# Performance work log

Measured on AMD Instinct MI355X. Metric: run time of the kernel, lower is better.

The kernel has to match this reference:

```python
import jax, jax.numpy as jnp
import numpy as np

N = 100000      # nodes
E = 1600000     # edges (avg degree 16)
DIN = 48        # input features
H = 48          # hidden
DOUT = 16       # output classes


def setup_inputs() -> dict:
    key = jax.random.key(0)
    ks = jax.random.split(key, 20)
    inp = {
        "x": jax.random.normal(ks[0], (N, DIN), jnp.float32),
        "edge_index": jax.random.randint(ks[1], (2, E), 0, N, jnp.int32),
    }
    # (name, in_dim, out_dim) for the 2-layer MLP in each of 3 GINConvs + final fc
    layers = [("11", DIN, H), ("12", H, H),
              ("21", H, H), ("22", H, H),
              ("31", H, H), ("32", H, H),
              ("f1", H, H), ("f2", H, DOUT)]
    for i, (nm, din, dout) in enumerate(layers):
        inp["w" + nm] = jax.random.normal(ks[2 + i], (din, dout), jnp.float32) / np.float32(np.sqrt(din))
        inp["b" + nm] = jax.random.normal(ks[10 + i], (dout,), jnp.float32) * 0.01
    return inp


def reference(x, edge_index, w11, b11, w12, b12, w21, b21, w22, b22,
              w31, b31, w32, b32, wf1, bf1, wf2, bf2):
    src, dst = edge_index[0], edge_index[1]
    n = x.shape[0]

    def gin_conv(h, w1, b1, w2, b2):
        # scatter-sum neighbor aggregation: sum_{j in N(i)} h_j
        agg = jax.ops.segment_sum(h[src], dst, num_segments=n)  # [N, d]
        h2 = h + agg  # eps = 0 (PyG GINConv default): (1+eps)*x + agg
        h2 = jax.nn.relu(h2 @ w1 + b1)
        return jax.nn.relu(h2 @ w2 + b2)

    h = gin_conv(x, w11, b11, w12, b12)
    h = gin_conv(h, w21, b21, w22, b22)
    h = gin_conv(h, w31, b31, w32, b32)
    # final fc head: Linear -> ReLU -> Linear
    return jax.nn.relu(h @ wf1 + bf1) @ wf2 + bf2
```

## Files before the change

kernel.cpp:

```cpp
#include <hip/hip_runtime.h>

#define NN 100000
#define NE 1600000
#define D 48
#define BK_SHIFT 8
#define BK_NODES 256
#define NBK 391
#define CAP 5120
#define EPB 4096
#define ST 72

typedef _Float16 f16x8 __attribute__((ext_vector_type(8)));
typedef _Float16 f16x2 __attribute__((ext_vector_type(2)));
typedef float f32x4 __attribute__((ext_vector_type(4)));


__global__ __launch_bounds__(256) void to_f16(const float* __restrict__ in,
                                              uint4* __restrict__ outh, int n8) {
    int i = blockIdx.x * 256 + threadIdx.x;
    if (i >= n8) return;
    const float4* p = (const float4*)(in + i * 8);
    float4 a = p[0], b = p[1];
    union { _Float16 h[8]; uint4 u; } pk;
    pk.h[0] = (_Float16)a.x; pk.h[1] = (_Float16)a.y;
    pk.h[2] = (_Float16)a.z; pk.h[3] = (_Float16)a.w;
    pk.h[4] = (_Float16)b.x; pk.h[5] = (_Float16)b.y;
    pk.h[6] = (_Float16)b.z; pk.h[7] = (_Float16)b.w;
    outh[i] = pk.u;
}


__global__ __launch_bounds__(256) void pack_weights(
    const float* __restrict__ w11, const float* __restrict__ w12,
    const float* __restrict__ w21, const float* __restrict__ w22,
    const float* __restrict__ w31, const float* __restrict__ w32,
    const float* __restrict__ wf1, const float* __restrict__ wf2,
    _Float16* __restrict__ wp) {
    int b = blockIdx.x;
    const float* W;
    int NL = 48;
    switch (b) {
        case 0: W = w11; break;
        case 1: W = w12; break;
        case 2: W = w21; break;
        case 3: W = w22; break;
        case 4: W = w31; break;
        case 5: W = w32; break;
        case 6: W = wf1; break;
        default: W = wf2; NL = 16; break;
    }
    _Float16* T = wp + b * 3072;
    int total = 64 * NL;
    for (int i = threadIdx.x; i < total; i += 256) {
        int j = i & 7;
        int m = i >> 3;
        int g = m / NL;
        int nn = m - g * NL;
        int k = g * 8 + j;
        T[i] = (k < 48) ? (_Float16)W[k * NL + nn] : (_Float16)0.f;
    }
}


__global__ __launch_bounds__(256) void bin_scatter(
    const int* __restrict__ src, const int* __restrict__ dst,
    int* __restrict__ bucketLen, int* __restrict__ arena) {
    __shared__ int sCnt[NBK];
    __shared__ int sBase[NBK];
    int tid = threadIdx.x;
    for (int i = tid; i < NBK; i += 256) sCnt[i] = 0;
    __syncthreads();
    int e0 = blockIdx.x * EPB;
    int eend = e0 + EPB;
    if (eend > NE) eend = NE;
    for (int i = e0 + tid; i < eend; i += 256) atomicAdd(&sCnt[dst[i] >> BK_SHIFT], 1);
    __syncthreads();
    for (int i = tid; i < NBK; i += 256) sBase[i] = atomicAdd(&bucketLen[i], sCnt[i]);
    __syncthreads();
    for (int i = tid; i < NBK; i += 256) sCnt[i] = 0;
    __syncthreads();
    for (int i = e0 + tid; i < eend; i += 256) {
        int d = dst[i];
        int b = d >> BK_SHIFT;
        int off = atomicAdd(&sCnt[b], 1) + sBase[b];
        if (off < CAP) arena[b * CAP + off] = ((d & (BK_NODES - 1)) << 17) | src[i];
    }
}

__global__ void scan_buckets(const int* __restrict__ bucketLen,
                             int* __restrict__ bucketBase, int* __restrict__ rowptr) {
    if (threadIdx.x == 0 && blockIdx.x == 0) {
        int s = 0;
        for (int b = 0; b < NBK; ++b) { bucketBase[b] = s; s += bucketLen[b]; }
        bucketBase[NBK] = s;
        rowptr[NN] = s;
    }
}


__global__ __launch_bounds__(256) void csr_from_bins(
    const int* __restrict__ arena, const int* __restrict__ bucketLen,
    const int* __restrict__ bucketBase, int* __restrict__ rowptr,
    int* __restrict__ colidx) {
    __shared__ int sCnt[BK_NODES];
    __shared__ int sTot[256];
    int b = blockIdx.x;
    int tid = threadIdx.x;
    int len = bucketLen[b];
    if (len > CAP) len = CAP;
    const int* ar = arena + b * CAP;
    int colBase = bucketBase[b];
    int nodeBase = b << BK_SHIFT;

    sCnt[tid] = 0;
    __syncthreads();
    for (int i = tid; i < len; i += 256) atomicAdd(&sCnt[ar[i] >> 17], 1);
    __syncthreads();

    int mine = sCnt[tid];
    sTot[tid] = mine;
    __syncthreads();
    for (int off = 1; off < 256; off <<= 1) {
        int add = 0;
        if (tid >= off) add = sTot[tid - off];
        __syncthreads();
        if (tid >= off) sTot[tid] += add;
        __syncthreads();
    }
    int excl = sTot[tid] - mine;
    int node = nodeBase + tid;
    if (node < NN) rowptr[node] = colBase + excl;
    __syncthreads();
    sCnt[tid] = colBase + excl;
    __syncthreads();
    for (int i = tid; i < len; i += 256) {
        int p = ar[i];
        int pos = atomicAdd(&sCnt[p >> 17], 1);
        colidx[pos] = p & 0x1FFFF;
    }
}


__global__ __launch_bounds__(256) void aggregate7(const unsigned* __restrict__ h16d,
                                                  const int* __restrict__ rowptr,
                                                  const int* __restrict__ col,
                                                  unsigned* __restrict__ outd, int n) {
    int wave = (blockIdx.x * 256 + threadIdx.x) >> 6;
    int lane = threadIdx.x & 63;
    if (wave >= n) return;
    int g = lane / 24;
    int c = lane - g * 24;
    int e0 = rowptr[wave];
    int e1 = rowptr[wave + 1];
    f16x2 acc = {0, 0};
    for (int eb = e0; eb < e1; eb += 8) {
#pragma unroll
        for (int u = 0; u < 4; ++u) {
            int ee = eb + u * 2 + g;
            bool ok = (g < 2) && (ee < e1);
            int s = col[ok ? ee : e0];
            unsigned v = h16d[(size_t)s * 24 + c];
            v = ok ? v : 0u;
            acc += *(const f16x2*)&v;
        }
    }
    unsigned au = *(const unsigned*)&acc;
    unsigned other = (unsigned)__shfl((int)au, c + 24);
    acc += *(const f16x2*)&other;
    if (g == 0) outd[(size_t)wave * 24 + c] = *(const unsigned*)&acc;
}


__device__ __forceinline__ void mfma_layer48(
    const _Float16* __restrict__ wp, const float* __restrict__ bias,
    const _Float16* src, _Float16* dst, int lane) {
    int am = lane & 15, q = lane >> 4;
    f16x8 a0 = *(const f16x8*)(src + am * ST + q * 8);
    f16x8 a1 = *(const f16x8*)(src + am * ST + 32 + q * 8);
#pragma unroll
    for (int t = 0; t < 3; ++t) {
        f16x8 b0 = *(const f16x8*)(wp + ((q) * 48 + t * 16 + am) * 8);
        f16x8 b1 = *(const f16x8*)(wp + ((4 + q) * 48 + t * 16 + am) * 8);
        float bv = bias[t * 16 + am];
        f32x4 c = {bv, bv, bv, bv};
        c = __builtin_amdgcn_mfma_f32_16x16x32_f16(a0, b0, c, 0, 0, 0);
        c = __builtin_amdgcn_mfma_f32_16x16x32_f16(a1, b1, c, 0, 0, 0);
#pragma unroll
        for (int r = 0; r < 4; ++r) {
            float v = fmaxf(c[r], 0.f);
            dst[(q * 4 + r) * ST + t * 16 + am] = (_Float16)v;
        }
    }
}

__device__ __forceinline__ void stage_mfma(const uint4* __restrict__ hin,
                                           const uint4* __restrict__ agg,
                                           _Float16* HA ,
                                           int base, int tid, int n) {
    for (int i = tid; i < 2 * 64 * 12; i += 256) {
        int b = i / (64 * 12);
        int rrow = (i / 12) % 64;
        int cc = i % 12;
        *(unsigned*)(HA + b * 64 * ST + rrow * ST + 48 + cc * 2) = 0u;
    }
    for (int i = tid; i < 64 * 6; i += 256) {
        int nl = i / 6, q = i - nl * 6;
        uint4 a = {0u, 0u, 0u, 0u};
        if (base + nl < n) {
            size_t gi = (size_t)(base + nl) * 6 + q;
            a = hin[gi];
            uint4 g = agg[gi];
            f16x8 s = *(const f16x8*)&a + *(const f16x8*)&g;
            a = *(const uint4*)&s;
        }
        *(uint4*)(HA + nl * ST + q * 8) = a;
    }
}

__global__ __launch_bounds__(256) void mlp2_mfma(
    const uint4* __restrict__ hin, const uint4* __restrict__ agg,
    const _Float16* __restrict__ wp1, const float* __restrict__ B1,
    const _Float16* __restrict__ wp2, const float* __restrict__ B2,
    _Float16* sh, int n) {
    __shared__ __align__(16) _Float16 HA[2 * 64 * ST];
    int tid = threadIdx.x;
    int base = blockIdx.x * 64;
    int lane = tid & 63;
    int wv = tid >> 6;

    stage_mfma(hin, agg, HA, base, tid, n);
    __syncthreads();

    const _Float16* s0 = HA + wv * 16 * ST;
    _Float16* s1 = HA + 64 * ST + wv * 16 * ST;
    mfma_layer48(wp1, B1, s0, s1, lane);

    int am = lane & 15, q = lane >> 4;
    f16x8 a0 = *(const f16x8*)(s1 + am * ST + q * 8);
    f16x8 a1 = *(const f16x8*)(s1 + am * ST + 32 + q * 8);
    int g0 = base + wv * 16;
#pragma unroll
    for (int t = 0; t < 3; ++t) {
        f16x8 b0 = *(const f16x8*)(wp2 + ((q) * 48 + t * 16 + am) * 8);
        f16x8 b1 = *(const f16x8*)(wp2 + ((4 + q) * 48 + t * 16 + am) * 8);
        float bv = B2[t * 16 + am];
        f32x4 c = {bv, bv, bv, bv};
        c = __builtin_amdgcn_mfma_f32_16x16x32_f16(a0, b0, c, 0, 0, 0);
        c = __builtin_amdgcn_mfma_f32_16x16x32_f16(a1, b1, c, 0, 0, 0);
#pragma unroll
        for (int r = 0; r < 4; ++r) {
            int node = g0 + q * 4 + r;
            if (node < n) {
                float v = fmaxf(c[r], 0.f);
                sh[(size_t)node * D + t * 16 + am] = (_Float16)v;
            }
        }
    }
}

__global__ __launch_bounds__(256) void mlp_tail_mfma(
    const uint4* __restrict__ hin, const uint4* __restrict__ agg,
    const _Float16* __restrict__ wp1, const float* __restrict__ B1,
    const _Float16* __restrict__ wp2, const float* __restrict__ B2,
    const _Float16* __restrict__ wp3, const float* __restrict__ B3,
    const _Float16* __restrict__ wp4, const float* __restrict__ B4,
    float* out, int n) {
    __shared__ __align__(16) _Float16 HA[2 * 64 * ST];
    int tid = threadIdx.x;
    int base = blockIdx.x * 64;
    int lane = tid & 63;
    int wv = tid >> 6;

    stage_mfma(hin, agg, HA, base, tid, n);
    __syncthreads();

    _Float16* s0 = HA + wv * 16 * ST;
    _Float16* s1 = HA + 64 * ST + wv * 16 * ST;
    mfma_layer48(wp1, B1, s0, s1, lane);
    mfma_layer48(wp2, B2, s1, s0, lane);
    mfma_layer48(wp3, B3, s0, s1, lane);

    int am = lane & 15, q = lane >> 4;
    f16x8 a0 = *(const f16x8*)(s1 + am * ST + q * 8);
    f16x8 a1 = *(const f16x8*)(s1 + am * ST + 32 + q * 8);
    f16x8 b0 = *(const f16x8*)(wp4 + ((q) * 16 + am) * 8);
    f16x8 b1 = *(const f16x8*)(wp4 + ((4 + q) * 16 + am) * 8);
    float bv = B4[am];
    f32x4 c = {bv, bv, bv, bv};
    c = __builtin_amdgcn_mfma_f32_16x16x32_f16(a0, b0, c, 0, 0, 0);
    c = __builtin_amdgcn_mfma_f32_16x16x32_f16(a1, b1, c, 0, 0, 0);
    int g0 = base + wv * 16;
#pragma unroll
    for (int r = 0; r < 4; ++r) {
        int node = g0 + q * 4 + r;
        if (node < n) out[(size_t)node * 16 + am] = c[r];
    }
}


extern "C" void kernel_launch(void* const* d_in, const int* in_sizes, int n_in,
                              void* d_out, int out_size, void* d_ws, size_t ws_size,
                              hipStream_t stream) {
    const int n = NN, e = NE;
    const float* x = (const float*)d_in[0];
    const int* ei = (const int*)d_in[1];
    const int* src = ei;
    const int* dst = ei + e;
    const float* w11 = (const float*)d_in[2];
    const float* b11 = (const float*)d_in[3];
    const float* w12 = (const float*)d_in[4];
    const float* b12 = (const float*)d_in[5];
    const float* w21 = (const float*)d_in[6];
    const float* b21 = (const float*)d_in[7];
    const float* w22 = (const float*)d_in[8];
    const float* b22 = (const float*)d_in[9];
    const float* w31 = (const float*)d_in[10];
    const float* b31 = (const float*)d_in[11];
    const float* w32 = (const float*)d_in[12];
    const float* b32 = (const float*)d_in[13];
    const float* wf1 = (const float*)d_in[14];
    const float* bf1 = (const float*)d_in[15];
    const float* wf2 = (const float*)d_in[16];
    const float* bf2 = (const float*)d_in[17];
    float* out = (float*)d_out;

    uint4* AG16 = (uint4*)d_ws;
    uint4* H16 = AG16 + (size_t)n * 6;
    _Float16* WP = (_Float16*)(H16 + (size_t)n * 6);
    int* rowptr = (int*)(WP + 8 * 3072);
    int* colidx = rowptr + (n + 1);
    int* arena = colidx + e;
    int* bucketLen = arena + (size_t)NBK * CAP;
    int* bucketBase = bucketLen + NBK;
    size_t needed = (size_t)((char*)(bucketBase + NBK + 1) - (char*)d_ws);
    if (needed > ws_size) return;

    const _Float16* wp11 = WP + 0 * 3072;
    const _Float16* wp12 = WP + 1 * 3072;
    const _Float16* wp21 = WP + 2 * 3072;
    const _Float16* wp22 = WP + 3 * 3072;
    const _Float16* wp31 = WP + 4 * 3072;
    const _Float16* wp32 = WP + 5 * 3072;
    const _Float16* wpf1 = WP + 6 * 3072;
    const _Float16* wpf2 = WP + 7 * 3072;

    hipMemsetAsync(bucketLen, 0, NBK * sizeof(int), stream);
    pack_weights<<<8, 256, 0, stream>>>(w11, w12, w21, w22, w31, w32, wf1, wf2, WP);
    to_f16<<<(n * 6 + 255) / 256, 256, 0, stream>>>(x, H16, n * 6);
    bin_scatter<<<(e + EPB - 1) / EPB, 256, 0, stream>>>(src, dst, bucketLen, arena);
    scan_buckets<<<1, 64, 0, stream>>>(bucketLen, bucketBase, rowptr);
    csr_from_bins<<<NBK, 256, 0, stream>>>(arena, bucketLen, bucketBase, rowptr, colidx);

    int gAgg = (n + 3) / 4;
    int gMlp = (n + 63) / 64;

    aggregate7<<<gAgg, 256, 0, stream>>>((const unsigned*)H16, rowptr, colidx, (unsigned*)AG16, n);
    mlp2_mfma<<<gMlp, 256, 0, stream>>>(H16, AG16, wp11, b11, wp12, b12, (_Float16*)H16, n);
    aggregate7<<<gAgg, 256, 0, stream>>>((const unsigned*)H16, rowptr, colidx, (unsigned*)AG16, n);
    mlp2_mfma<<<gMlp, 256, 0, stream>>>(H16, AG16, wp21, b21, wp22, b22, (_Float16*)H16, n);
    aggregate7<<<gAgg, 256, 0, stream>>>((const unsigned*)H16, rowptr, colidx, (unsigned*)AG16, n);
    mlp_tail_mfma<<<gMlp, 256, 0, stream>>>(H16, AG16, wp31, b31, wp32, b32,
                                            wpf1, bf1, wpf2, bf2, out, n);
}
```

Baseline: 320.8 us.

## Fuse neighbor aggregation into MLP kernels and merge prep launches

Folds the CSR gather-sum directly into each GIN conv MLP kernel: each wave aggregates its 16 nodes into LDS, then runs the MFMA layers. This drops the intermediate aggregate buffer round-trip and three launches, and uses ping-pong feature buffers. It also merges weight packing, bucket zeroing and the x-to-f16 conversion into one prep kernel, and replaces the serial bucket scan with a parallel LDS scan. The risk is lower gather parallelism, since one wave now walks 16 nodes serially instead of one node per wave, which can hurt latency hiding.

Measured after the change: 287.6 us. -10.3%, faster.

```diff
diff --git a/kernel.cpp b/kernel.cpp
--- a/kernel.cpp
+++ b/kernel.cpp
@@ -15,49 +15,53 @@
 typedef float f32x4 __attribute__((ext_vector_type(4)));
 
 
-__global__ __launch_bounds__(256) void to_f16(const float* __restrict__ in,
-                                              uint4* __restrict__ outh, int n8) {
-    int i = blockIdx.x * 256 + threadIdx.x;
-    if (i >= n8) return;
-    const float4* p = (const float4*)(in + i * 8);
-    float4 a = p[0], b = p[1];
-    union { _Float16 h[8]; uint4 u; } pk;
-    pk.h[0] = (_Float16)a.x; pk.h[1] = (_Float16)a.y;
-    pk.h[2] = (_Float16)a.z; pk.h[3] = (_Float16)a.w;
-    pk.h[4] = (_Float16)b.x; pk.h[5] = (_Float16)b.y;
-    pk.h[6] = (_Float16)b.z; pk.h[7] = (_Float16)b.w;
-    outh[i] = pk.u;
-}
-
-
-__global__ __launch_bounds__(256) void pack_weights(
+__global__ __launch_bounds__(256) void prep(
+    const float* __restrict__ x,
     const float* __restrict__ w11, const float* __restrict__ w12,
     const float* __restrict__ w21, const float* __restrict__ w22,
     const float* __restrict__ w31, const float* __restrict__ w32,
     const float* __restrict__ wf1, const float* __restrict__ wf2,
-    _Float16* __restrict__ wp) {
+    _Float16* __restrict__ wp, uint4* __restrict__ outh,
+    int* __restrict__ bucketLen) {
     int b = blockIdx.x;
-    const float* W;
-    int NL = 48;
-    switch (b) {
-        case 0: W = w11; break;
-        case 1: W = w12; break;
-        case 2: W = w21; break;
-        case 3: W = w22; break;
-        case 4: W = w31; break;
-        case 5: W = w32; break;
-        case 6: W = wf1; break;
-        default: W = wf2; NL = 16; break;
-    }
-    _Float16* T = wp + b * 3072;
-    int total = 64 * NL;
-    for (int i = threadIdx.x; i < total; i += 256) {
-        int j = i & 7;
-        int m = i >> 3;
-        int g = m / NL;
-        int nn = m - g * NL;
-        int k = g * 8 + j;
-        T[i] = (k < 48) ? (_Float16)W[k * NL + nn] : (_Float16)0.f;
+    int tid = threadIdx.x;
+    if (b < 8) {
+        const float* W;
+        int NL = 48;
+        switch (b) {
+            case 0: W = w11; break;
+            case 1: W = w12; break;
+            case 2: W = w21; break;
+            case 3: W = w22; break;
+            case 4: W = w31; break;
+            case 5: W = w32; break;
+            case 6: W = wf1; break;
+            default: W = wf2; NL = 16; break;
+        }
+        _Float16* T = wp + b * 3072;
+        int total = 64 * NL;
+        for (int i = tid; i < total; i += 256) {
+            int j = i & 7;
+            int m = i >> 3;
+            int g = m / NL;
+            int nn = m - g * NL;
+            int k = g * 8 + j;
+            T[i] = (k < 48) ? (_Float16)W[k * NL + nn] : (_Float16)0.f;
+        }
+    } else if (b == 8) {
+        for (int i = tid; i < NBK; i += 256) bucketLen[i] = 0;
+    } else {
+        int i = (b - 9) * 256 + tid;
+        if (i < NN * 6) {
+            const float4* p = (const float4*)(x + (size_t)i * 8);
+            float4 a = p[0], bb = p[1];
+            union { _Float16 h[8]; uint4 u; } pk;
+            pk.h[0] = (_Float16)a.x; pk.h[1] = (_Float16)a.y;
+            pk.h[2] = (_Float16)a.z; pk.h[3] = (_Float16)a.w;
+            pk.h[4] = (_Float16)bb.x; pk.h[5] = (_Float16)bb.y;
+            pk.h[6] = (_Float16)bb.z; pk.h[7] = (_Float16)bb.w;
+            outh[i] = pk.u;
+        }
     }
 }
 
@@ -87,13 +91,25 @@
     }
 }
 
-__global__ void scan_buckets(const int* __restrict__ bucketLen,
-                             int* __restrict__ bucketBase, int* __restrict__ rowptr) {
-    if (threadIdx.x == 0 && blockIdx.x == 0) {
-        int s = 0;
-        for (int b = 0; b < NBK; ++b) { bucketBase[b] = s; s += bucketLen[b]; }
-        bucketBase[NBK] = s;
-        rowptr[NN] = s;
+
+__global__ __launch_bounds__(512) void scan_buckets_par(
+    const int* __restrict__ bucketLen, int* __restrict__ bucketBase,
+    int* __restrict__ rowptr) {
+    __shared__ int s[512];
+    int t = threadIdx.x;
+    int mine = (t < NBK) ? bucketLen[t] : 0;
+    s[t] = mine;
+    __syncthreads();
+    for (int off = 1; off < 512; off <<= 1) {
+        int v = (t >= off) ? s[t - off] : 0;
+        __syncthreads();
+        s[t] += v;
+        __syncthreads();
+    }
+    if (t < NBK) bucketBase[t] = s[t] - mine;
+    if (t == NBK - 1) {
+        bucketBase[NBK] = s[t];
+        rowptr[NN] = s[t];
     }
 }
 
@@ -141,36 +157,6 @@
 }
 
 
-__global__ __launch_bounds__(256) void aggregate7(const unsigned* __restrict__ h16d,
-                                                  const int* __restrict__ rowptr,
-                                                  const int* __restrict__ col,
-                                                  unsigned* __restrict__ outd, int n) {
-    int wave = (blockIdx.x * 256 + threadIdx.x) >> 6;
-    int lane = threadIdx.x & 63;
-    if (wave >= n) return;
-    int g = lane / 24;
-    int c = lane - g * 24;
-    int e0 = rowptr[wave];
-    int e1 = rowptr[wave + 1];
-    f16x2 acc = {0, 0};
-    for (int eb = e0; eb < e1; eb += 8) {
-#pragma unroll
-        for (int u = 0; u < 4; ++u) {
-            int ee = eb + u * 2 + g;
-            bool ok = (g < 2) && (ee < e1);
-            int s = col[ok ? ee : e0];
-            unsigned v = h16d[(size_t)s * 24 + c];
-            v = ok ? v : 0u;
-            acc += *(const f16x2*)&v;
-        }
-    }
-    unsigned au = *(const unsigned*)&acc;
-    unsigned other = (unsigned)__shfl((int)au, c + 24);
-    acc += *(const f16x2*)&other;
-    if (g == 0) outd[(size_t)wave * 24 + c] = *(const unsigned*)&acc;
-}
-
-
 __device__ __forceinline__ void mfma_layer48(
     const _Float16* __restrict__ wp, const float* __restrict__ bias,
     const _Float16* src, _Float16* dst, int lane) {
@@ -193,47 +179,70 @@
     }
 }
 
-__device__ __forceinline__ void stage_mfma(const uint4* __restrict__ hin,
-                                           const uint4* __restrict__ agg,
-                                           _Float16* HA ,
-                                           int base, int tid, int n) {
-    for (int i = tid; i < 2 * 64 * 12; i += 256) {
-        int b = i / (64 * 12);
-        int rrow = (i / 12) % 64;
-        int cc = i % 12;
-        *(unsigned*)(HA + b * 64 * ST + rrow * ST + 48 + cc * 2) = 0u;
-    }
-    for (int i = tid; i < 64 * 6; i += 256) {
-        int nl = i / 6, q = i - nl * 6;
-        uint4 a = {0u, 0u, 0u, 0u};
-        if (base + nl < n) {
-            size_t gi = (size_t)(base + nl) * 6 + q;
-            a = hin[gi];
-            uint4 g = agg[gi];
-            f16x8 s = *(const f16x8*)&a + *(const f16x8*)&g;
-            a = *(const uint4*)&s;
-        }
-        *(uint4*)(HA + nl * ST + q * 8) = a;
-    }
-}
-
-__global__ __launch_bounds__(256) void mlp2_mfma(
-    const uint4* __restrict__ hin, const uint4* __restrict__ agg,
+
+__device__ __forceinline__ void gather_stage(const unsigned* __restrict__ hin,
+                                             const int* __restrict__ rowptr,
+                                             const int* __restrict__ col,
+                                             _Float16* s0, _Float16* s1,
+                                             int base, int wv, int lane, int n) {
+    for (int i = lane; i < 16 * 12; i += 64) {
+        int r = i / 12, cdw = i % 12;
+        *(unsigned*)(s0 + r * ST + 48 + cdw * 2) = 0u;
+        *(unsigned*)(s1 + r * ST + 48 + cdw * 2) = 0u;
+    }
+    int g = lane / 24;
+    int c = lane - g * 24;
+    for (int nl = 0; nl < 16; ++nl) {
+        int node = base + wv * 16 + nl;
+        f16x2 acc = {0, 0};
+        if (node < n) {
+            int e0 = rowptr[node];
+            int e1 = rowptr[node + 1];
+            for (int eb = e0; eb < e1; eb += 16) {
+#pragma unroll
+                for (int u = 0; u < 8; ++u) {
+                    int ee = eb + u * 2 + g;
+                    bool ok = (g < 2) && (ee < e1);
+                    int s = col[ok ? ee : e0];
+                    unsigned v = hin[(size_t)s * 24 + c];
+                    v = ok ? v : 0u;
+                    acc += *(const f16x2*)&v;
+                }
+            }
+        }
+        unsigned au = *(const unsigned*)&acc;
+        unsigned other = (unsigned)__shfl((int)au, c + 24);
+        acc += *(const f16x2*)&other;
+        if (g == 0) {
+            unsigned res = 0u;
+            if (node < n) {
+                unsigned self = hin[(size_t)node * 24 + c];
+                acc += *(const f16x2*)&self;
+                res = *(const unsigned*)&acc;
+            }
+            *(unsigned*)(s0 + nl * ST + c * 2) = res;
+        }
+    }
+    __builtin_amdgcn_wave_barrier();
+}
+
+__global__ __launch_bounds__(256) void conv_fused(
+    const unsigned* __restrict__ hin, const int* __restrict__ rowptr,
+    const int* __restrict__ col,
     const _Float16* __restrict__ wp1, const float* __restrict__ B1,
     const _Float16* __restrict__ wp2, const float* __restrict__ B2,
-    _Float16* sh, int n) {
+    _Float16* __restrict__ hout, int n) {
     __shared__ __align__(16) _Float16 HA[2 * 64 * ST];
     int tid = threadIdx.x;
     int base = blockIdx.x * 64;
     int lane = tid & 63;
     int wv = tid >> 6;
-
-    stage_mfma(hin, agg, HA, base, tid, n);
-    __syncthreads();
-
-    const _Float16* s0 = HA + wv * 16 * ST;
+    _Float16* s0 = HA + wv * 16 * ST;
     _Float16* s1 = HA + 64 * ST + wv * 16 * ST;
+
+    gather_stage(hin, rowptr, col, s0, s1, base, wv, lane, n);
     mfma_layer48(wp1, B1, s0, s1, lane);
+    __builtin_amdgcn_wave_barrier();
 
     int am = lane & 15, q = lane >> 4;
     f16x8 a0 = *(const f16x8*)(s1 + am * ST + q * 8);
@@ -252,33 +261,35 @@
             int node = g0 + q * 4 + r;
             if (node < n) {
                 float v = fmaxf(c[r], 0.f);
-                sh[(size_t)node * D + t * 16 + am] = (_Float16)v;
+                hout[(size_t)node * D + t * 16 + am] = (_Float16)v;
             }
         }
     }
 }
 
-__global__ __launch_bounds__(256) void mlp_tail_mfma(
-    const uint4* __restrict__ hin, const uint4* __restrict__ agg,
+__global__ __launch_bounds__(256) void tail_fused(
+    const unsigned* __restrict__ hin, const int* __restrict__ rowptr,
+    const int* __restrict__ col,
     const _Float16* __restrict__ wp1, const float* __restrict__ B1,
     const _Float16* __restrict__ wp2, const float* __restrict__ B2,
     const _Float16* __restrict__ wp3, const float* __restrict__ B3,
     const _Float16* __restrict__ wp4, const float* __restrict__ B4,
-    float* out, int n) {
+    float* __restrict__ out, int n) {
     __shared__ __align__(16) _Float16 HA[2 * 64 * ST];
     int tid = threadIdx.x;
     int base = blockIdx.x * 64;
     int lane = tid & 63;
     int wv = tid >> 6;
-
-    stage_mfma(hin, agg, HA, base, tid, n);
-    __syncthreads();
-
     _Float16* s0 = HA + wv * 16 * ST;
     _Float16* s1 = HA + 64 * ST + wv * 16 * ST;
+
+    gather_stage(hin, rowptr, col, s0, s1, base, wv, lane, n);
     mfma_layer48(wp1, B1, s0, s1, lane);
+    __builtin_amdgcn_wave_barrier();
     mfma_layer48(wp2, B2, s1, s0, lane);
+    __builtin_amdgcn_wave_barrier();
     mfma_layer48(wp3, B3, s0, s1, lane);
+    __builtin_amdgcn_wave_barrier();
 
     int am = lane & 15, q = lane >> 4;
     f16x8 a0 = *(const f16x8*)(s1 + am * ST + q * 8);
@@ -324,9 +335,9 @@
     const float* bf2 = (const float*)d_in[17];
     float* out = (float*)d_out;
 
-    uint4* AG16 = (uint4*)d_ws;
-    uint4* H16 = AG16 + (size_t)n * 6;
-    _Float16* WP = (_Float16*)(H16 + (size_t)n * 6);
+    uint4* HAa = (uint4*)d_ws;
+    uint4* HAb = HAa + (size_t)n * 6;
+    _Float16* WP = (_Float16*)(HAb + (size_t)n * 6);
     int* rowptr = (int*)(WP + 8 * 3072);
     int* colidx = rowptr + (n + 1);
     int* arena = colidx + e;
@@ -344,21 +355,20 @@
     const _Float16* wpf1 = WP + 6 * 3072;
     const _Float16* wpf2 = WP + 7 * 3072;
 
-    hipMemsetAsync(bucketLen, 0, NBK * sizeof(int), stream);
-    pack_weights<<<8, 256, 0, stream>>>(w11, w12, w21, w22, w31, w32, wf1, wf2, WP);
-    to_f16<<<(n * 6 + 255) / 256, 256, 0, stream>>>(x, H16, n * 6);
+    int gPrep = 9 + (n * 6 + 255) / 256;
+    prep<<<gPrep, 256, 0, stream>>>(x, w11, w12, w21, w22, w31, w32, wf1, wf2,
+                                    WP, HAa, bucketLen);
     bin_scatter<<<(e + EPB - 1) / EPB, 256, 0, stream>>>(src, dst, bucketLen, arena);
-    scan_buckets<<<1, 64, 0, stream>>>(bucketLen, bucketBase, rowptr);
+    scan_buckets_par<<<1, 512, 0, stream>>>(bucketLen, bucketBase, rowptr);
     csr_from_bins<<<NBK, 256, 0, stream>>>(arena, bucketLen, bucketBase, rowptr, colidx);
 
-    int gAgg = (n + 3) / 4;
-    int gMlp = (n + 63) / 64;
-
-    aggregate7<<<gAgg, 256, 0, stream>>>((const unsigned*)H16, rowptr, colidx, (unsigned*)AG16, n);
-    mlp2_mfma<<<gMlp, 256, 0, stream>>>(H16, AG16, wp11, b11, wp12, b12, (_Float16*)H16, n);
-    aggregate7<<<gAgg, 256, 0, stream>>>((const unsigned*)H16, rowptr, colidx, (unsigned*)AG16, n);
-    mlp2_mfma<<<gMlp, 256, 0, stream>>>(H16, AG16, wp21, b21, wp22, b22, (_Float16*)H16, n);
-    aggregate7<<<gAgg, 256, 0, stream>>>((const unsigned*)H16, rowptr, colidx, (unsigned*)AG16, n);
-    mlp_tail_mfma<<<gMlp, 256, 0, stream>>>(H16, AG16, wp31, b31, wp32, b32,
-                                            wpf1, bf1, wpf2, bf2, out, n);
-}
+    int gConv = (n + 63) / 64;
+
+    conv_fused<<<gConv, 256, 0, stream>>>((const unsigned*)HAa, rowptr, colidx,
+                                          wp11, b11, wp12, b12, (_Float16*)HAb, n);
+    conv_fused<<<gConv, 256, 0, stream>>>((const unsigned*)HAb, rowptr, colidx,
+                                          wp21, b21, wp22, b22, (_Float16*)HAa, n);
+    tail_fused<<<gConv, 256, 0, stream>>>((const unsigned*)HAa, rowptr, colidx,
+                                          wp31, b31, wp32, b32,
+                                          wpf1, bf1, wpf2, bf2, out, n);
+}
```
